# Optimization experiments

Measured on AMD Instinct MI355X. Metric: run time of the kernel, lower is better.

## Reference

```python
import jax, jax.numpy as jnp
import numpy as np

N, D, DH, H = 2048, 256, 256, 4
DHEAD = DH // H
NEG = -1e30


def setup_inputs() -> dict:
    key = jax.random.key(0)
    ks = jax.random.split(key, 24)
    s = 0.05
    inp = {
        'axiom_states': jax.random.normal(ks[0], (N, D), jnp.float32),
        'adj0': (jax.random.uniform(ks[1], (N, N)) < 0.015).astype(jnp.float32),
        'adj1': (jax.random.uniform(ks[2], (N, N)) < 0.015).astype(jnp.float32),
        'w0': jax.random.uniform(ks[3], (N, N), jnp.float32),
        'w1': jax.random.uniform(ks[4], (N, N), jnp.float32),
        'Wm0': jax.random.normal(ks[5], (DH, D), jnp.float32) * s,
        'bm0': jax.random.normal(ks[6], (DH,), jnp.float32) * s,
        'Wa0': jax.random.normal(ks[7], (H, 2 * D), jnp.float32) * s,
        'ba0': jax.random.normal(ks[8], (H,), jnp.float32) * s,
        'Wm1': jax.random.normal(ks[9], (DH, D), jnp.float32) * s,
        'bm1': jax.random.normal(ks[10], (DH,), jnp.float32) * s,
        'Wa1': jax.random.normal(ks[11], (H, 2 * D), jnp.float32) * s,
        'ba1': jax.random.normal(ks[12], (H,), jnp.float32) * s,
        'gru_wih': jax.random.normal(ks[13], (3 * D, 2 * DH), jnp.float32) * s,
        'gru_whh': jax.random.normal(ks[14], (3 * D, D), jnp.float32) * s,
        'gru_bih': jax.random.normal(ks[15], (3 * D,), jnp.float32) * s,
        'gru_bhh': jax.random.normal(ks[16], (3 * D,), jnp.float32) * s,
        'ln_g': jnp.ones((D,), jnp.float32),
        'ln_b': jnp.zeros((D,), jnp.float32),
    }
    return inp


def _edge_messages(x, adj, w, Wm, bm, Wa, ba):
    # GAT-style decomposition of Linear([x_i, x_j]) -> a_cur[i] + a_nb[j] + b
    a_cur = x @ Wa[:, :D].T                      # [N,H] (target i, first half of concat)
    a_nb = x @ Wa[:, D:].T                       # [N,H] (neighbor j, second half)
    s = a_nb[:, None, :] + a_cur[None, :, :] + ba  # [j,i,H]
    s = jax.nn.leaky_relu(s, 0.2)
    s = s * w[:, :, None]                        # edge-weight scaled scores (pre-softmax)
    mask = adj != 0                              # edge j -> i iff adj[j,i] != 0
    logits = jnp.where(mask[:, :, None], s, NEG)
    attn = jax.nn.softmax(logits, axis=0) * mask[:, :, None]  # zero for isolated nodes
    msg = (x @ Wm.T + bm).reshape(N, H, DHEAD)   # per-neighbor messages
    agg = jnp.einsum('jih,jhd->ihd', attn, msg)  # softmax-weighted sum over neighbors
    return agg.reshape(N, DH)


def _forward(axiom_states, adj0, adj1, w0, w1, Wm0, bm0, Wa0, ba0,
             Wm1, bm1, Wa1, ba1, gru_wih, gru_whh, gru_bih, gru_bhh, ln_g, ln_b):
    m0 = _edge_messages(axiom_states, adj0, w0, Wm0, bm0, Wa0, ba0)
    m1 = _edge_messages(axiom_states, adj1, w1, Wm1, bm1, Wa1, ba1)
    msg = jnp.concatenate([m0, m1], axis=-1)     # dropout is identity in eval
    # GRUCell (torch semantics)
    gi = msg @ gru_wih.T + gru_bih
    gh = axiom_states @ gru_whh.T + gru_bhh
    r = jax.nn.sigmoid(gi[:, :D] + gh[:, :D])
    z = jax.nn.sigmoid(gi[:, D:2 * D] + gh[:, D:2 * D])
    n = jnp.tanh(gi[:, 2 * D:] + r * gh[:, 2 * D:])
    h = (1.0 - z) * n + z * axiom_states
    # LayerNorm
    mu = jnp.mean(h, axis=-1, keepdims=True)
    var = jnp.var(h, axis=-1, keepdims=True)
    return (h - mu) * jax.lax.rsqrt(var + 1e-5) * ln_g + ln_b


def reference(axiom_states, adj0, adj1, w0, w1, Wm0, bm0, Wa0, ba0,
              Wm1, bm1, Wa1, ba1, gru_wih, gru_whh, gru_bih, gru_bhh, ln_g, ln_b):
    return _forward(axiom_states, adj0, adj1, w0, w1, Wm0, bm0, Wa0, ba0,
                    Wm1, bm1, Wa1, ba1, gru_wih, gru_whh, gru_bih, gru_bhh, ln_g, ln_b)
```

## Files before the change

### kernel.cpp

```cpp
#include <hip/hip_runtime.h>

#define NN 2048
#define DD 256
#define HH 4
#define PW 1280
#define ECAP 128

typedef unsigned short ushort_t;
typedef __attribute__((ext_vector_type(8))) short s8;
typedef __attribute__((ext_vector_type(4))) float f4;

__device__ __forceinline__ ushort_t f2b(float f) {
    unsigned int u = __float_as_uint(f);
    return (ushort_t)((u + 0x7fffu + ((u >> 16) & 1u)) >> 16);
}
__device__ __forceinline__ float b2f(ushort_t b) {
    return __uint_as_float(((unsigned int)b) << 16);
}
__device__ __forceinline__ void gl_lds16(const void* g, void* l) {
    __builtin_amdgcn_global_load_lds(
        (const __attribute__((address_space(1))) void*)g,
        (__attribute__((address_space(3))) void*)l, 16, 0, 0);
}

#define NB_CONV 4885

__global__ __launch_bounds__(256) void prep_kernel(
    const float* __restrict__ x, const float* __restrict__ Wm0, const float* __restrict__ Wm1,
    const float* __restrict__ whh, const float* __restrict__ wih,
    const float* __restrict__ bm0, const float* __restrict__ bm1, const float* __restrict__ bhh,
    const float* __restrict__ Wa0, const float* __restrict__ Wa1,
    ushort_t* __restrict__ xb, ushort_t* __restrict__ Wcatb, ushort_t* __restrict__ wihb,
    float* __restrict__ bcat, int* __restrict__ cnt,
    float* __restrict__ acur, float* __restrict__ anb)
{
    __shared__ float xs[16][257];
    const int t = threadIdx.x;
    if (blockIdx.x < NB_CONV) {
        int id = blockIdx.x * 256 + t;
        if (id < NN * DD) { xb[id] = f2b(x[id]); return; }
        id -= NN * DD;
        if (id < PW * DD) {
            const int c = id >> 8, k = id & 255;
            const float v = (c < 256) ? Wm0[c * DD + k]
                          : (c < 512) ? Wm1[(c - 256) * DD + k]
                                      : whh[(c - 512) * DD + k];
            Wcatb[id] = f2b(v); return;
        }
        id -= PW * DD;
        if (id < 768 * 512) { wihb[id] = f2b(wih[id]); return; }
        id -= 768 * 512;
        if (id < PW) {
            bcat[id] = (id < 256) ? bm0[id] : (id < 512) ? bm1[id - 256] : bhh[id - 512];
            return;
        }
        id -= PW;
        if (id < 2 * NN) cnt[id] = 0;
        return;
    }
    const int i0 = (blockIdx.x - NB_CONV) * 16;
    for (int rr = 0; rr < 16; ++rr)
        xs[rr][t] = x[(size_t)(i0 + rr) * DD + t];
    __syncthreads();
    const int r = t >> 4, idx = t & 15;
    const int l = idx >> 3, isnb = (idx >> 2) & 1, h = idx & 3;
    const float* wrow = (l ? Wa1 : Wa0) + h * (2 * DD) + isnb * DD;
    float acc = 0.f;
    for (int k = 0; k < DD; ++k) acc = fmaf(xs[r][k], wrow[k], acc);
    float* dst = isnb ? anb : acur;
    dst[((size_t)l * NN + i0 + r) * HH + h] = acc;
}

__global__ __launch_bounds__(256) void gemm_mfma(
    const ushort_t* __restrict__ A, const ushort_t* __restrict__ B,
    const float* __restrict__ bias,
    float* __restrict__ Cf, ushort_t* __restrict__ Cb,
    int lda, int ldb, int ldc, int K, int split)
{
    __shared__ ushort_t as[64][64];
    __shared__ ushort_t bs[64][64];
    const int t = threadIdx.x;
    const int wave = t >> 6, lane = t & 63;
    const int r0 = blockIdx.y * 64, c0 = blockIdx.x * 64;
    const int wm = (wave & 1) * 32, wn = (wave >> 1) * 32;
    const int fm = lane & 15, fq = lane >> 4;

    const int m0q0 = wave * 16 + (lane >> 3);
    const int m0q1 = m0q0 + 8;
    const int cs0 = ((lane & 7) ^ (m0q0 & 7)) * 8;
    const int cs1 = ((lane & 7) ^ (m0q1 & 7)) * 8;
    const ushort_t* ga0 = A + (size_t)(r0 + m0q0) * lda + cs0;
    const ushort_t* ga1 = A + (size_t)(r0 + m0q1) * lda + cs1;
    const ushort_t* gb0 = B + (size_t)(c0 + m0q0) * ldb + cs0;
    const ushort_t* gb1 = B + (size_t)(c0 + m0q1) * ldb + cs1;
    ushort_t* la0 = &as[wave * 16][0];
    ushort_t* la1 = &as[wave * 16 + 8][0];
    ushort_t* lb0 = &bs[wave * 16][0];
    ushort_t* lb1 = &bs[wave * 16 + 8][0];

    const int ra0 = wm + fm, ra1 = wm + 16 + fm;
    const int rb0 = wn + fm, rb1 = wn + 16 + fm;

    f4 acc[2][2] = {};

    for (int k0 = 0; k0 < K; k0 += 64) {
        __syncthreads();
        gl_lds16(ga0 + k0, la0);
        gl_lds16(ga1 + k0, la1);
        gl_lds16(gb0 + k0, lb0);
        gl_lds16(gb1 + k0, lb1);
        __syncthreads();
        #pragma unroll
        for (int kk = 0; kk < 2; ++kk) {
            const int cc = kk * 4 + fq;
            const s8 a0 = *(const s8*)&as[ra0][(cc ^ (ra0 & 7)) * 8];
            const s8 a1 = *(const s8*)&as[ra1][(cc ^ (ra1 & 7)) * 8];
            const s8 b0 = *(const s8*)&bs[rb0][(cc ^ (rb0 & 7)) * 8];
            const s8 b1 = *(const s8*)&bs[rb1][(cc ^ (rb1 & 7)) * 8];
            acc[0][0] = __builtin_amdgcn_mfma_f32_16x16x32_bf16(a0, b0, acc[0][0], 0, 0, 0);
            acc[0][1] = __builtin_amdgcn_mfma_f32_16x16x32_bf16(a0, b1, acc[0][1], 0, 0, 0);
            acc[1][0] = __builtin_amdgcn_mfma_f32_16x16x32_bf16(a1, b0, acc[1][0], 0, 0, 0);
            acc[1][1] = __builtin_amdgcn_mfma_f32_16x16x32_bf16(a1, b1, acc[1][1], 0, 0, 0);
        }
    }
    #pragma unroll
    for (int ni = 0; ni < 2; ++ni) {
        const int col = c0 + wn + ni * 16 + fm;
        const float bv = bias[col];
        #pragma unroll
        for (int mi = 0; mi < 2; ++mi) {
            #pragma unroll
            for (int r = 0; r < 4; ++r) {
                const int row = r0 + wm + mi * 16 + fq * 4 + r;
                const float v = acc[mi][ni][r] + bv;
                if (!split) {
                    Cf[(size_t)row * ldc + col] = v;
                } else if (col < 512) {
                    Cb[(size_t)row * 512 + col] = f2b(v);
                } else {
                    Cf[(size_t)row * 768 + col - 512] = v;
                }
            }
        }
    }
}

__global__ __launch_bounds__(256) void edge_build(
    const float* __restrict__ adj0, const float* __restrict__ adj1,
    const float* __restrict__ w0, const float* __restrict__ w1,
    int* __restrict__ cnt, int* __restrict__ ej, float* __restrict__ ew)
{
    const int j = blockIdx.x, l = blockIdx.y, t = threadIdx.x;
    const float* adj = l ? adj1 : adj0;
    const float* w   = l ? w1 : w0;
    #pragma unroll
    for (int it = 0; it < 2; ++it) {
        const int i4 = (t + it * 256) * 4;
        const float4 a = *(const float4*)(adj + (size_t)j * NN + i4);
        const float av[4] = {a.x, a.y, a.z, a.w};
        #pragma unroll
        for (int u = 0; u < 4; ++u) {
            if (av[u] != 0.f) {
                const int i = i4 + u;
                const int slot = atomicAdd(&cnt[l * NN + i], 1);
                if (slot < ECAP) {
                    const size_t base = ((size_t)l * NN + i) * ECAP + slot;
                    ej[base] = j;
                    ew[base] = w[(size_t)j * NN + i];
                }
            }
        }
    }
}

__global__ __launch_bounds__(256) void attn_kernel(
    const int* __restrict__ cnt, const int* __restrict__ ej, const float* __restrict__ ew,
    const float* __restrict__ acur, const float* __restrict__ anb,
    const float* __restrict__ ba0, const float* __restrict__ ba1,
    const ushort_t* __restrict__ msgb, ushort_t* __restrict__ mcatb)
{
    const int i = blockIdx.x, l = blockIdx.y, t = threadIdx.x;
    __shared__ float es[HH][ECAP];
    __shared__ int ejs[ECAP];
    const int ne = min(cnt[l * NN + i], ECAP);
    const float* ba = l ? ba1 : ba0;
    const size_t ebase = ((size_t)l * NN + i) * ECAP;

    if (t < ne) {
        const int j = ej[ebase + t];
        const float wv = ew[ebase + t];
        ejs[t] = j;
        const float4 av = *(const float4*)(anb + ((size_t)l * NN + j) * HH);
        const float sv[4] = {av.x, av.y, av.z, av.w};
        #pragma unroll
        for (int h = 0; h < HH; ++h) {
            float s = sv[h] + acur[((size_t)l * NN + i) * HH + h] + ba[h];
            s = (s > 0.f) ? s : 0.2f * s;
            es[h][t] = s * wv;
        }
    }
    __syncthreads();
    {
        const int h = t >> 6, lane = t & 63;
        float s0 = (lane < ne) ? es[h][lane] : -1e30f;
        float s1 = (lane + 64 < ne) ? es[h][lane + 64] : -1e30f;
        float m = fmaxf(s0, s1);
        #pragma unroll
        for (int off = 32; off; off >>= 1) m = fmaxf(m, __shfl_xor(m, off));
        const float p0 = expf(s0 - m), p1 = expf(s1 - m);
        float sum = p0 + p1;
        #pragma unroll
        for (int off = 32; off; off >>= 1) sum += __shfl_xor(sum, off);
        const float inv = (ne > 0) ? 1.f / sum : 0.f;
        es[h][lane] = p0 * inv;
        if (lane + 64 < ECAP) es[h][lane + 64] = p1 * inv;
    }
    __syncthreads();
    const int h = t >> 6;
    const int off = l * DD + t;
    float acc = 0.f;
    int e = 0;
    for (; e + 4 <= ne; e += 4) {
        const float v0 = b2f(msgb[(size_t)ejs[e + 0] * 512 + off]);
        const float v1 = b2f(msgb[(size_t)ejs[e + 1] * 512 + off]);
        const float v2 = b2f(msgb[(size_t)ejs[e + 2] * 512 + off]);
        const float v3 = b2f(msgb[(size_t)ejs[e + 3] * 512 + off]);
        acc = fmaf(es[h][e + 0], v0, acc);
        acc = fmaf(es[h][e + 1], v1, acc);
        acc = fmaf(es[h][e + 2], v2, acc);
        acc = fmaf(es[h][e + 3], v3, acc);
    }
    for (; e < ne; ++e)
        acc = fmaf(es[h][e], b2f(msgb[(size_t)ejs[e] * 512 + off]), acc);
    mcatb[(size_t)i * (2 * DD) + off] = f2b(acc);
}

__global__ __launch_bounds__(256) void gates_ln(
    const float* __restrict__ gi, const float* __restrict__ gh, const float* __restrict__ x,
    const float* __restrict__ lng, const float* __restrict__ lnb, float* __restrict__ out)
{
    __shared__ float rs1[4], rs2[4];
    const int t = threadIdx.x;
    const int r0 = blockIdx.x * 4;
    const float gv = lng[t], bv = lnb[t];
    float hv[4];
    #pragma unroll
    for (int r = 0; r < 4; ++r) {
        const int row = r0 + r;
        const float gir = gi[(size_t)row * 768 + t];
        const float giz = gi[(size_t)row * 768 + 256 + t];
        const float gin = gi[(size_t)row * 768 + 512 + t];
        const float ghr = gh[(size_t)row * 768 + t];
        const float ghz = gh[(size_t)row * 768 + 256 + t];
        const float ghn = gh[(size_t)row * 768 + 512 + t];
        const float rr = 1.f / (1.f + expf(-(gir + ghr)));
        const float zz = 1.f / (1.f + expf(-(giz + ghz)));
        const float nn = tanhf(gin + rr * ghn);
        hv[r] = (1.f - zz) * nn + zz * x[(size_t)row * DD + t];
    }
    const int lane = t & 63, wid = t >> 6;
    for (int r = 0; r < 4; ++r) {
        float s1 = hv[r], s2 = hv[r] * hv[r];
        #pragma unroll
        for (int off = 32; off; off >>= 1) {
            s1 += __shfl_down(s1, off);
            s2 += __shfl_down(s2, off);
        }
        if (lane == 0) { rs1[wid] = s1; rs2[wid] = s2; }
        __syncthreads();
        const float sum = rs1[0] + rs1[1] + rs1[2] + rs1[3];
        const float sq  = rs2[0] + rs2[1] + rs2[2] + rs2[3];
        const float mu  = sum * (1.f / DD);
        const float var = sq * (1.f / DD) - mu * mu;
        const float inv = rsqrtf(var + 1e-5f);
        out[(size_t)(r0 + r) * DD + t] = (hv[r] - mu) * inv * gv + bv;
        __syncthreads();
    }
}

extern "C" void kernel_launch(void* const* d_in, const int* in_sizes, int n_in,
                              void* d_out, int out_size, void* d_ws, size_t ws_size,
                              hipStream_t stream)
{
    const float* x    = (const float*)d_in[0];
    const float* adj0 = (const float*)d_in[1];
    const float* adj1 = (const float*)d_in[2];
    const float* w0   = (const float*)d_in[3];
    const float* w1   = (const float*)d_in[4];
    const float* Wm0  = (const float*)d_in[5];
    const float* bm0  = (const float*)d_in[6];
    const float* Wa0  = (const float*)d_in[7];
    const float* ba0  = (const float*)d_in[8];
    const float* Wm1  = (const float*)d_in[9];
    const float* bm1  = (const float*)d_in[10];
    const float* Wa1  = (const float*)d_in[11];
    const float* ba1  = (const float*)d_in[12];
    const float* wih  = (const float*)d_in[13];
    const float* whh  = (const float*)d_in[14];
    const float* bih  = (const float*)d_in[15];
    const float* bhh  = (const float*)d_in[16];
    const float* lng  = (const float*)d_in[17];
    const float* lnb  = (const float*)d_in[18];
    float* out = (float*)d_out;

    float* ws = (float*)d_ws;
    float* gh   = ws;            ws += (size_t)NN * 768;
    float* gi   = ws;            ws += (size_t)NN * 768;
    float* bcat = ws;            ws += PW;
    float* acur = ws;            ws += 2 * NN * HH;
    float* anb  = ws;            ws += 2 * NN * HH;
    int*   cnt  = (int*)ws;      ws += 2 * NN;
    int*   ej   = (int*)ws;      ws += 2 * NN * ECAP;
    float* ew   = ws;            ws += 2 * NN * ECAP;
    ushort_t* xb    = (ushort_t*)ws;  ws += (size_t)NN * DD / 2;
    ushort_t* Wcatb = (ushort_t*)ws;  ws += (size_t)PW * DD / 2;
    ushort_t* wihb  = (ushort_t*)ws;  ws += (size_t)768 * 512 / 2;
    ushort_t* msgb  = (ushort_t*)ws;  ws += (size_t)NN * 512 / 2;
    ushort_t* mcatb = (ushort_t*)ws;  ws += (size_t)NN * 512 / 2;

    prep_kernel<<<NB_CONV + NN / 16, 256, 0, stream>>>(
        x, Wm0, Wm1, whh, wih, bm0, bm1, bhh, Wa0, Wa1,
        xb, Wcatb, wihb, bcat, cnt, acur, anb);
    gemm_mfma<<<dim3(PW / 64, NN / 64), 256, 0, stream>>>(
        xb, Wcatb, bcat, gh, msgb, DD, DD, 0, DD, 1);
    edge_build<<<dim3(NN, 2), 256, 0, stream>>>(adj0, adj1, w0, w1, cnt, ej, ew);
    attn_kernel<<<dim3(NN, 2), 256, 0, stream>>>(cnt, ej, ew, acur, anb, ba0, ba1, msgb, mcatb);
    gemm_mfma<<<dim3(768 / 64, NN / 64), 256, 0, stream>>>(
        mcatb, wihb, bih, gi, (ushort_t*)nullptr, 2 * DD, 2 * DD, 768, 2 * DD, 0);
    gates_ln<<<NN / 4, 256, 0, stream>>>(gi, gh, x, lng, lnb, out);
}
```

Before: 200.3 us.

## Fuse edge-list build into prep kernel and vectorize bf16 conversions

Edge-list construction from the adjacency matrices moves into the prep kernel, with the counter zeroing split into a tiny separate kernel that runs first. The fp32-to-bf16 conversions now process four elements per thread with float4 loads and packed stores. The bias-concatenation buffer is removed by selecting biases directly in specialized GEMM epilogues. This targets launch overhead and serialization between edge building and the other prep work, at the cost of an extra small launch and a larger heterogeneous kernel.

After: 206.5 us. 1.03x slower.

```diff
diff --git a/kernel.cpp b/kernel.cpp
--- a/kernel.cpp
+++ b/kernel.cpp
@@ -7,6 +7,7 @@
 #define ECAP 128
 
 typedef unsigned short ushort_t;
+typedef __attribute__((ext_vector_type(4))) unsigned short us4;
 typedef __attribute__((ext_vector_type(8))) short s8;
 typedef __attribute__((ext_vector_type(4))) float f4;
 
@@ -23,65 +24,102 @@
         (__attribute__((address_space(3))) void*)l, 16, 0, 0);
 }
 
-#define NB_CONV 4885
+__global__ __launch_bounds__(256) void zero_cnt(int* __restrict__ cnt)
+{
+    const int id = blockIdx.x * 256 + threadIdx.x;
+    if (id < 2 * NN) cnt[id] = 0;
+}
+
+#define K1_EB  4096
+#define K1_XC  4608
+#define K1_WC  4928
+#define K1_WI  5312
+#define K1_NB  5440
 
 __global__ __launch_bounds__(256) void prep_kernel(
-    const float* __restrict__ x, const float* __restrict__ Wm0, const float* __restrict__ Wm1,
+    const float* __restrict__ x,
+    const float* __restrict__ adj0, const float* __restrict__ adj1,
+    const float* __restrict__ w0, const float* __restrict__ w1,
+    const float* __restrict__ Wm0, const float* __restrict__ Wm1,
     const float* __restrict__ whh, const float* __restrict__ wih,
-    const float* __restrict__ bm0, const float* __restrict__ bm1, const float* __restrict__ bhh,
     const float* __restrict__ Wa0, const float* __restrict__ Wa1,
+    int* __restrict__ cnt, int* __restrict__ ej, float* __restrict__ ew,
     ushort_t* __restrict__ xb, ushort_t* __restrict__ Wcatb, ushort_t* __restrict__ wihb,
-    float* __restrict__ bcat, int* __restrict__ cnt,
     float* __restrict__ acur, float* __restrict__ anb)
 {
-    __shared__ float xs[16][257];
-    const int t = threadIdx.x;
-    if (blockIdx.x < NB_CONV) {
-        int id = blockIdx.x * 256 + t;
-        if (id < NN * DD) { xb[id] = f2b(x[id]); return; }
-        id -= NN * DD;
-        if (id < PW * DD) {
-            const int c = id >> 8, k = id & 255;
-            const float v = (c < 256) ? Wm0[c * DD + k]
-                          : (c < 512) ? Wm1[(c - 256) * DD + k]
-                                      : whh[(c - 512) * DD + k];
-            Wcatb[id] = f2b(v); return;
-        }
-        id -= PW * DD;
-        if (id < 768 * 512) { wihb[id] = f2b(wih[id]); return; }
-        id -= 768 * 512;
-        if (id < PW) {
-            bcat[id] = (id < 256) ? bm0[id] : (id < 512) ? bm1[id - 256] : bhh[id - 512];
-            return;
-        }
-        id -= PW;
-        if (id < 2 * NN) cnt[id] = 0;
+    __shared__ float sh[16][257];
+    const int b = blockIdx.x, t = threadIdx.x;
+
+    if (b < K1_EB) {
+        const int j = b & 2047, l = b >> 11;
+        const float* adj = l ? adj1 : adj0;
+        const float* w   = l ? w1 : w0;
+        #pragma unroll
+        for (int it = 0; it < 2; ++it) {
+            const int i4 = (t + it * 256) * 4;
+            const float4 a = *(const float4*)(adj + (size_t)j * NN + i4);
+            const float av[4] = {a.x, a.y, a.z, a.w};
+            #pragma unroll
+            for (int u = 0; u < 4; ++u) {
+                if (av[u] != 0.f) {
+                    const int i = i4 + u;
+                    const int slot = atomicAdd(&cnt[l * NN + i], 1);
+                    if (slot >= 0 && slot < ECAP) {
+                        const size_t base = ((size_t)l * NN + i) * ECAP + slot;
+                        ej[base] = j;
+                        ew[base] = w[(size_t)j * NN + i];
+                    }
+                }
+            }
+        }
         return;
     }
-    const int i0 = (blockIdx.x - NB_CONV) * 16;
-    for (int rr = 0; rr < 16; ++rr)
-        xs[rr][t] = x[(size_t)(i0 + rr) * DD + t];
-    __syncthreads();
-    const int r = t >> 4, idx = t & 15;
-    const int l = idx >> 3, isnb = (idx >> 2) & 1, h = idx & 3;
-    const float* wrow = (l ? Wa1 : Wa0) + h * (2 * DD) + isnb * DD;
-    float acc = 0.f;
-    for (int k = 0; k < DD; ++k) acc = fmaf(xs[r][k], wrow[k], acc);
-    float* dst = isnb ? anb : acur;
-    dst[((size_t)l * NN + i0 + r) * HH + h] = acc;
-}
-
-__global__ __launch_bounds__(256) void gemm_mfma(
-    const ushort_t* __restrict__ A, const ushort_t* __restrict__ B,
-    const float* __restrict__ bias,
-    float* __restrict__ Cf, ushort_t* __restrict__ Cb,
-    int lda, int ldb, int ldc, int K, int split)
-{
-    __shared__ ushort_t as[64][64];
-    __shared__ ushort_t bs[64][64];
+    if (b < K1_XC) {
+        const int id = (b - K1_EB) * 1024 + t * 4;
+        const float4 v = *(const float4*)(x + id);
+        us4 o; o.x = f2b(v.x); o.y = f2b(v.y); o.z = f2b(v.z); o.w = f2b(v.w);
+        *(us4*)(xb + id) = o;
+        return;
+    }
+    if (b < K1_WC) {
+        const int id = (b - K1_XC) * 1024 + t * 4;
+        const int c = id >> 8, k = id & 255;
+        const float* src = (c < 256) ? Wm0 + (size_t)c * DD + k
+                         : (c < 512) ? Wm1 + (size_t)(c - 256) * DD + k
+                                     : whh + (size_t)(c - 512) * DD + k;
+        const float4 v = *(const float4*)src;
+        us4 o; o.x = f2b(v.x); o.y = f2b(v.y); o.z = f2b(v.z); o.w = f2b(v.w);
+        *(us4*)(Wcatb + id) = o;
+        return;
+    }
+    if (b < K1_WI) {
+        const int id = (b - K1_WC) * 1024 + t * 4;
+        const float4 v = *(const float4*)(wih + id);
+        us4 o; o.x = f2b(v.x); o.y = f2b(v.y); o.z = f2b(v.z); o.w = f2b(v.w);
+        *(us4*)(wihb + id) = o;
+        return;
+    }
+    {
+        const int i0 = (b - K1_WI) * 16;
+        for (int rr = 0; rr < 16; ++rr)
+            sh[rr][t] = x[(size_t)(i0 + rr) * DD + t];
+        __syncthreads();
+        const int r = t >> 4, idx = t & 15;
+        const int l = idx >> 3, isnb = (idx >> 2) & 1, h = idx & 3;
+        const float* wrow = (l ? Wa1 : Wa0) + h * (2 * DD) + isnb * DD;
+        float acc = 0.f;
+        for (int k = 0; k < DD; ++k) acc = fmaf(sh[r][k], wrow[k], acc);
+        float* dst = isnb ? anb : acur;
+        dst[((size_t)l * NN + i0 + r) * HH + h] = acc;
+    }
+}
+
+__device__ __forceinline__ void gemm_core(
+    const ushort_t* __restrict__ A, int lda, const ushort_t* __restrict__ B, int ldb,
+    int r0, int c0, int K, ushort_t (*as)[64], ushort_t (*bs)[64], f4 acc[2][2])
+{
     const int t = threadIdx.x;
     const int wave = t >> 6, lane = t & 63;
-    const int r0 = blockIdx.y * 64, c0 = blockIdx.x * 64;
     const int wm = (wave & 1) * 32, wn = (wave >> 1) * 32;
     const int fm = lane & 15, fq = lane >> 4;
 
@@ -97,11 +135,8 @@
     ushort_t* la1 = &as[wave * 16 + 8][0];
     ushort_t* lb0 = &bs[wave * 16][0];
     ushort_t* lb1 = &bs[wave * 16 + 8][0];
-
     const int ra0 = wm + fm, ra1 = wm + 16 + fm;
     const int rb0 = wn + fm, rb1 = wn + 16 + fm;
-
-    f4 acc[2][2] = {};
 
     for (int k0 = 0; k0 < K; k0 += 64) {
         __syncthreads();
@@ -123,51 +158,37 @@
             acc[1][1] = __builtin_amdgcn_mfma_f32_16x16x32_bf16(a1, b1, acc[1][1], 0, 0, 0);
         }
     }
+}
+
+__global__ __launch_bounds__(256) void gemm1_kernel(
+    const ushort_t* __restrict__ xb, const ushort_t* __restrict__ Wcatb,
+    const float* __restrict__ bm0, const float* __restrict__ bm1,
+    const float* __restrict__ bhh,
+    ushort_t* __restrict__ msgb, float* __restrict__ gh)
+{
+    __shared__ ushort_t as[64][64];
+    __shared__ ushort_t bs[64][64];
+    const int t = threadIdx.x;
+    const int wave = t >> 6, lane = t & 63;
+    const int wm = (wave & 1) * 32, wn = (wave >> 1) * 32;
+    const int fm = lane & 15, fq = lane >> 4;
+    const int c0 = blockIdx.x * 64, r0 = blockIdx.y * 64;
+    f4 acc[2][2] = {};
+    gemm_core(xb, DD, Wcatb, DD, r0, c0, DD, as, bs, acc);
     #pragma unroll
     for (int ni = 0; ni < 2; ++ni) {
         const int col = c0 + wn + ni * 16 + fm;
-        const float bv = bias[col];
+        const float bv = (col < 256) ? bm0[col]
+                       : (col < 512) ? bm1[col - 256]
+                                     : bhh[col - 512];
         #pragma unroll
         for (int mi = 0; mi < 2; ++mi) {
             #pragma unroll
             for (int r = 0; r < 4; ++r) {
                 const int row = r0 + wm + mi * 16 + fq * 4 + r;
                 const float v = acc[mi][ni][r] + bv;
-                if (!split) {
-                    Cf[(size_t)row * ldc + col] = v;
-                } else if (col < 512) {
-                    Cb[(size_t)row * 512 + col] = f2b(v);
-                } else {
-                    Cf[(size_t)row * 768 + col - 512] = v;
-                }
-            }
-        }
-    }
-}
-
-__global__ __launch_bounds__(256) void edge_build(
-    const float* __restrict__ adj0, const float* __restrict__ adj1,
-    const float* __restrict__ w0, const float* __restrict__ w1,
-    int* __restrict__ cnt, int* __restrict__ ej, float* __restrict__ ew)
-{
-    const int j = blockIdx.x, l = blockIdx.y, t = threadIdx.x;
-    const float* adj = l ? adj1 : adj0;
-    const float* w   = l ? w1 : w0;
-    #pragma unroll
-    for (int it = 0; it < 2; ++it) {
-        const int i4 = (t + it * 256) * 4;
-        const float4 a = *(const float4*)(adj + (size_t)j * NN + i4);
-        const float av[4] = {a.x, a.y, a.z, a.w};
-        #pragma unroll
-        for (int u = 0; u < 4; ++u) {
-            if (av[u] != 0.f) {
-                const int i = i4 + u;
-                const int slot = atomicAdd(&cnt[l * NN + i], 1);
-                if (slot < ECAP) {
-                    const size_t base = ((size_t)l * NN + i) * ECAP + slot;
-                    ej[base] = j;
-                    ew[base] = w[(size_t)j * NN + i];
-                }
+                if (col < 512) msgb[(size_t)row * 512 + col] = f2b(v);
+                else           gh[(size_t)row * 768 + col - 512] = v;
             }
         }
     }
@@ -182,7 +203,7 @@
     const int i = blockIdx.x, l = blockIdx.y, t = threadIdx.x;
     __shared__ float es[HH][ECAP];
     __shared__ int ejs[ECAP];
-    const int ne = min(cnt[l * NN + i], ECAP);
+    const int ne = min(max(cnt[l * NN + i], 0), ECAP);
     const float* ba = l ? ba1 : ba0;
     const size_t ebase = ((size_t)l * NN + i) * ECAP;
 
@@ -233,6 +254,32 @@
     for (; e < ne; ++e)
         acc = fmaf(es[h][e], b2f(msgb[(size_t)ejs[e] * 512 + off]), acc);
     mcatb[(size_t)i * (2 * DD) + off] = f2b(acc);
+}
+
+__global__ __launch_bounds__(256) void gemm2_kernel(
+    const ushort_t* __restrict__ mcatb, const ushort_t* __restrict__ wihb,
+    const float* __restrict__ bih, float* __restrict__ gi)
+{
+    __shared__ ushort_t as[64][64];
+    __shared__ ushort_t bs[64][64];
+    const int t = threadIdx.x;
+    const int wave = t >> 6, lane = t & 63;
+    const int wm = (wave & 1) * 32, wn = (wave >> 1) * 32;
+    const int fm = lane & 15, fq = lane >> 4;
+    const int c0 = blockIdx.x * 64, r0 = blockIdx.y * 64;
+    f4 acc[2][2] = {};
+    gemm_core(mcatb, 512, wihb, 512, r0, c0, 512, as, bs, acc);
+    #pragma unroll
+    for (int ni = 0; ni < 2; ++ni) {
+        const int col = c0 + wn + ni * 16 + fm;
+        const float bv = bih[col];
+        #pragma unroll
+        for (int mi = 0; mi < 2; ++mi)
+            #pragma unroll
+            for (int r = 0; r < 4; ++r)
+                gi[(size_t)(r0 + wm + mi * 16 + fq * 4 + r) * 768 + col] =
+                    acc[mi][ni][r] + bv;
+    }
 }
 
 __global__ __launch_bounds__(256) void gates_ln(
@@ -306,7 +353,6 @@
     float* ws = (float*)d_ws;
     float* gh   = ws;            ws += (size_t)NN * 768;
     float* gi   = ws;            ws += (size_t)NN * 768;
-    float* bcat = ws;            ws += PW;
     float* acur = ws;            ws += 2 * NN * HH;
     float* anb  = ws;            ws += 2 * NN * HH;
     int*   cnt  = (int*)ws;      ws += 2 * NN;
@@ -318,14 +364,14 @@
     ushort_t* msgb  = (ushort_t*)ws;  ws += (size_t)NN * 512 / 2;
     ushort_t* mcatb = (ushort_t*)ws;  ws += (size_t)NN * 512 / 2;
 
-    prep_kernel<<<NB_CONV + NN / 16, 256, 0, stream>>>(
-        x, Wm0, Wm1, whh, wih, bm0, bm1, bhh, Wa0, Wa1,
-        xb, Wcatb, wihb, bcat, cnt, acur, anb);
-    gemm_mfma<<<dim3(PW / 64, NN / 64), 256, 0, stream>>>(
-        xb, Wcatb, bcat, gh, msgb, DD, DD, 0, DD, 1);
-    edge_build<<<dim3(NN, 2), 256, 0, stream>>>(adj0, adj1, w0, w1, cnt, ej, ew);
-    attn_kernel<<<dim3(NN, 2), 256, 0, stream>>>(cnt, ej, ew, acur, anb, ba0, ba1, msgb, mcatb);
-    gemm_mfma<<<dim3(768 / 64, NN / 64), 256, 0, stream>>>(
-        mcatb, wihb, bih, gi, (ushort_t*)nullptr, 2 * DD, 2 * DD, 768, 2 * DD, 0);
+    zero_cnt<<<16, 256, 0, stream>>>(cnt);
+    prep_kernel<<<K1_NB, 256, 0, stream>>>(
+        x, adj0, adj1, w0, w1, Wm0, Wm1, whh, wih, Wa0, Wa1,
+        cnt, ej, ew, xb, Wcatb, wihb, acur, anb);
+    gemm1_kernel<<<dim3(PW / 64, NN / 64), 256, 0, stream>>>(
+        xb, Wcatb, bm0, bm1, bhh, msgb, gh);
+    attn_kernel<<<dim3(NN, 2), 256, 0, stream>>>(
+        cnt, ej, ew, acur, anb, ba0, ba1, msgb, mcatb);
+    gemm2_kernel<<<dim3(12, 32), 256, 0, stream>>>(mcatb, wihb, bih, gi);
     gates_ln<<<NN / 4, 256, 0, stream>>>(gi, gh, x, lng, lnb, out);
 }
```
